# Optimization experiments

Measured on AMD Instinct MI355X. Metric: run time of the kernel, lower is better.

The kernel has to match this reference:

```python
import jax, jax.numpy as jnp
import numpy as np

EPS = 1e-5

def _sqnorm(x):
    return jnp.sum(x * x, axis=-1, keepdims=True)

def _norm(x):
    return jnp.sqrt(_sqnorm(x) + 1e-15)

def _artanh(x):
    return jnp.arctanh(jnp.clip(x, -1.0 + EPS, 1.0 - EPS))

def exp0(v):
    n = _norm(v)
    return jnp.tanh(n) * v / jnp.maximum(n, EPS)

def log0(x):
    n = jnp.clip(_norm(x), EPS, 1.0 - EPS)
    return _artanh(n) * x / n

def mob_scalar(x, r):
    n = jnp.clip(_norm(x), EPS, 1.0 - EPS)
    return jnp.tanh(r * _artanh(n)) * x / n

def mob_add(x, y):
    x2 = _sqnorm(x); y2 = _sqnorm(y)
    xy = jnp.sum(x * y, axis=-1, keepdims=True)
    num = (1.0 + 2.0 * xy + y2) * x + (1.0 - x2) * y
    den = 1.0 + 2.0 * xy + x2 * y2
    return num / jnp.maximum(den, EPS)

def pdist(x, y):
    # Poincare-ball geodesic distance, keepdims on last axis
    d2 = _sqnorm(x - y)
    den = jnp.maximum((1.0 - _sqnorm(x)) * (1.0 - _sqnorm(y)), EPS)
    return jnp.arccosh(jnp.maximum(1.0 + 2.0 * d2 / den, 1.0 + 1e-7))

def _coattention(D, Q, q1):
    # vectorized form of the per-slot loop: each slot i reads the ORIGINAL D[:, i]
    Dd = jax.lax.stop_gradient(D)                       # Zk_s is detached in torch
    # [N, F_D, F_Q, 1] attention over Q neighbors for every D slot
    G = jax.nn.softmax(-pdist(Dd[:, :, None, :], Q[:, None, :, :]), axis=2)
    nh = exp0(jnp.sum(log0(mob_scalar(Q[:, None, :, :], G)), axis=2))  # [N, F_D, d]
    return mob_add(mob_scalar(Dd, q1), nh)

def _aggregate(h_self, h_neigh, scalar):
    att = jax.nn.softmax(-pdist(h_self[:, None, :], h_neigh), axis=1)  # [N, F, 1]
    nTE = exp0(jnp.sum(log0(mob_scalar(h_neigh, att)), axis=1))        # [N, d]
    return mob_add(mob_scalar(h_self, scalar), nTE)

def _mode_forward(x, D_idx, Q_idx, emb0, emb1, win, bin_, q, qq, q1, aw1, ab1, aw2, wout, bout):
    f = jnp.concatenate([emb0[x[:, 0]], emb1[x[:, 1]]], axis=-1)  # [N, 64]
    f = exp0(f @ win + bin_)
    D = f[D_idx]; Q = f[Q_idx]                                    # [N, F, d]
    h_neigh = _coattention(D, Q, q1)
    e1 = _aggregate(f, h_neigh, q)
    e2 = _aggregate(f, Q, qq)
    z = jnp.stack([log0(e1), log0(e2)], axis=1)                   # [N, 2, d]
    beta = jax.nn.softmax(jnp.tanh(z @ aw1 + ab1) @ aw2, axis=1)  # [N, 2, 1]
    rst = exp0(jnp.sum(beta * z, axis=1))
    return exp0(log0(rst) @ wout + bout)

N, F, DH, V0, V1 = 2048, 20, 64, 100000, 1000

def setup_inputs() -> dict:
    key = jax.random.key(0)
    ks = jax.random.split(key, 32)
    def mk(k, shape, s=0.1):
        return (jax.random.normal(k, shape) * s).astype(jnp.float32)
    inp = {
        'x': jax.random.randint(ks[0], (N, 2), 0, V1).astype(jnp.int32),
        'idx_sim': jax.random.randint(ks[1], (N, F), 0, N).astype(jnp.int32),
        'idx_cor': jax.random.randint(ks[2], (N, F), 0, N).astype(jnp.int32),
    }
    for mi, m in enumerate(['sim', 'cor']):
        kk = jax.random.split(ks[3 + mi], 12)
        inp[f'emb0_{m}'] = mk(kk[0], (V0, 32))
        inp[f'emb1_{m}'] = mk(kk[1], (V1, 32))
        inp[f'win_{m}'] = mk(kk[2], (64, DH))
        inp[f'bin_{m}'] = mk(kk[3], (DH,))
        inp[f'q_{m}'] = jnp.full((1,), 0.1, jnp.float32)
        inp[f'qq_{m}'] = jnp.full((1,), 0.1, jnp.float32)
        inp[f'q1_{m}'] = jnp.full((1,), 0.1, jnp.float32)
        inp[f'aw1_{m}'] = mk(kk[4], (64, 32))
        inp[f'ab1_{m}'] = mk(kk[5], (32,))
        inp[f'aw2_{m}'] = mk(kk[6], (32, 1))
        inp[f'wout_{m}'] = mk(kk[7], (DH, 64))
        inp[f'bout_{m}'] = mk(kk[8], (64,))
    return inp

def reference(x, idx_sim, idx_cor,
              emb0_sim, emb1_sim, win_sim, bin_sim, q_sim, qq_sim, q1_sim,
              aw1_sim, ab1_sim, aw2_sim, wout_sim, bout_sim,
              emb0_cor, emb1_cor, win_cor, bin_cor, q_cor, qq_cor, q1_cor,
              aw1_cor, ab1_cor, aw2_cor, wout_cor, bout_cor):
    # mode 'sim': D = feat[idx_cor], Q = feat[idx_sim]; mode 'cor': swapped
    out_sim = _mode_forward(x, idx_cor, idx_sim, emb0_sim, emb1_sim, win_sim, bin_sim,
                            q_sim, qq_sim, q1_sim, aw1_sim, ab1_sim, aw2_sim, wout_sim, bout_sim)
    out_cor = _mode_forward(x, idx_sim, idx_cor, emb0_cor, emb1_cor, win_cor, bin_cor,
                            q_cor, qq_cor, q1_cor, aw1_cor, ab1_cor, aw2_cor, wout_cor, bout_cor)
    return jnp.stack([out_sim, out_cor], axis=0)  # [2, N, 64]
```

## Files before the change

kernel.cpp:

```cpp
#include <hip/hip_runtime.h>

#define EPS 1e-5f
#define ONE_M_EPS (1.0f - 1e-5f)
#define NROW 2048
#define FF 20
#define DH 64
#define PADW (DH + 4)
#define NPAIR (FF * FF)
#define NPAIR2 (NPAIR + FF)

typedef float v2f __attribute__((ext_vector_type(2)));

__device__ __forceinline__ float frcp(float x) { return __builtin_amdgcn_rcpf(x); }
__device__ __forceinline__ float fsq(float x) { return __builtin_amdgcn_sqrtf(x); }
__device__ __forceinline__ v2f pkfma(v2f a, v2f b, v2f c) {
  return __builtin_elementwise_fma(a, b, c);
}

template <int CTRL>
__device__ __forceinline__ float dppadd(float x) {
  int t = __builtin_amdgcn_update_dpp(0, __float_as_int(x), CTRL, 0xf, 0xf, false);
  return x + __int_as_float(t);
}
__device__ __forceinline__ float wredb(float v) {
  v = dppadd<0x111>(v);
  v = dppadd<0x112>(v);
  v = dppadd<0x114>(v);
  v = dppadd<0x118>(v);
  v = dppadd<0x142>(v);
  v = dppadd<0x143>(v);
  return __int_as_float(__builtin_amdgcn_readlane(__float_as_int(v), 63));
}

__device__ __forceinline__ float ftanh(float x) {
  float ax = fabsf(x);
  float e = __expf(-2.f * ax);
  float t = (1.f - e) * frcp(1.f + e);
  return copysignf(t, x);
}

__device__ __forceinline__ float ftanhp(float x) {
  float e = __expf(-2.f * x);
  return (1.f - e) * frcp(1.f + e);
}

__device__ __forceinline__ float fatanh(float x) {
  return 0.5f * __logf((1.f + x) * frcp(1.f - x));
}

__device__ __forceinline__ float clampn(float x) {
  return fminf(fmaxf(x, EPS), ONE_M_EPS);
}

__device__ __forceinline__ float expnacosh(float arg) {
  return frcp(arg + fsq(fmaxf(arg * arg - 1.f, 0.f)));
}

__device__ __forceinline__ float dot64(const float* __restrict__ a,
                                       const float* __restrict__ b) {
  const float4* ap = (const float4*)a;
  const float4* bp = (const float4*)b;
  v2f acc = {0.f, 0.f};
#pragma unroll
  for (int kk = 0; kk < DH / 4; ++kk) {
    float4 x = ap[kk];
    float4 y = bp[kk];
    acc = pkfma(v2f{x.x, x.y}, v2f{y.x, y.y}, acc);
    acc = pkfma(v2f{x.z, x.w}, v2f{y.z, y.w}, acc);
  }
  return acc.x + acc.y;
}

struct FeatParams {
  const float *emb0, *emb1, *win, *bin;
  float* fout;
};

struct ModeParams {
  const float* f;
  const int *Didx, *Qidx;
  const float *q1p, *qp, *qqp, *aw1, *ab1, *aw2, *wout, *bout;
  float* out;
};

__global__ __launch_bounds__(64) void feat_kernel(const int* __restrict__ x,
                                                  FeatParams ps, FeatParams pc) {
  const int bid = blockIdx.x;
  const int mode = bid >= NROW;
  const FeatParams P = mode ? pc : ps;
  const int n = bid - mode * NROW;
  const int l = threadIdx.x;
  __shared__ float u[DH];
  int x0 = x[n * 2 + 0];
  int x1 = x[n * 2 + 1];
  u[l] = (l < 32) ? P.emb0[x0 * 32 + l] : P.emb1[x1 * 32 + (l - 32)];
  __syncthreads();
  v2f acc2 = {P.bin[l], 0.f};
#pragma unroll
  for (int k = 0; k < DH; k += 2) {
    v2f uv = *(const v2f*)&u[k];
    v2f wv = {P.win[k * DH + l], P.win[(k + 1) * DH + l]};
    acc2 = pkfma(uv, wv, acc2);
  }
  float acc = acc2.x + acc2.y;
  float a2 = wredb(acc * acc);
  float nn = fsq(a2 + 1e-15f);
  P.fout[n * DH + l] = ftanhp(nn) * frcp(fmaxf(nn, EPS)) * acc;
}

__global__ __launch_bounds__(256, 4) void mode_kernel(ModeParams pm0,
                                                      ModeParams pm1) {
  const int bid = blockIdx.x;
  const int mode = bid >= NROW;
  const ModeParams P = mode ? pm1 : pm0;
  const int n = bid - mode * NROW;
  const int tid = threadIdx.x;
  const int l = tid & 63;
  const int w = tid >> 6;

  __shared__ alignas(16) float Ds[FF][PADW];
  __shared__ alignas(16) float Qs[FF][PADW];
  __shared__ alignas(16) float fs_[PADW];
  __shared__ alignas(16) float Gm[NPAIR];
  __shared__ float Fq[FF];
  __shared__ float D2[FF];
  __shared__ float FD[FF], X2s[FF];
  __shared__ float Q2[FF], WQ[FF];
  __shared__ float zb[2][DH];
  __shared__ float ub[DH];
  __shared__ float pb[4][DH];

  const float* f = P.f;
  float fv = f[n * DH + l];

  for (int i = w; i < FF; i += 4) {
    Ds[i][l] = f[P.Didx[n * FF + i] * DH + l];
    Qs[i][l] = f[P.Qidx[n * FF + i] * DH + l];
  }
  if (w == 0) fs_[l] = fv;
  float f2 = wredb(fv * fv);
  float fnc = clampn(fsq(f2 + 1e-15f));
  float fA = fatanh(fnc);
  float q1 = P.q1p[0], qsc = P.qp[0], qqsc = P.qqp[0];
  __syncthreads();

  if (w < 2 && l < FF) {
    const float* rp = (w == 0) ? &Ds[l][0] : &Qs[l][0];
    float dot = dot64(rp, rp);
    float nc = clampn(fsq(dot + 1e-15f));
    float at = fatanh(nc);
    if (w == 0) {
      D2[l] = dot;
      float fd = ftanh(q1 * at) * frcp(nc);
      FD[l] = fd;
      X2s[l] = fd * fd * dot;
    } else {
      Q2[l] = dot;
      WQ[l] = at * frcp(nc);
    }
  }
  __syncthreads();

  float qregS[FF];
#pragma unroll
  for (int j = 0; j < FF; ++j) qregS[j] = WQ[j] * Qs[j][l];

  for (int p = tid; p < NPAIR2; p += 256) {
    int i = p / FF;
    int j = p - i * FF;
    const float* ap = (i < FF) ? &Ds[i][0] : &fs_[0];
    float dot = dot64(ap, &Qs[j][0]);
    if (i < FF) {
      float d2 = D2[i] + Q2[j] - 2.f * dot;
      float den = fmaxf((1.f - D2[i]) * (1.f - Q2[j]), EPS);
      float arg = fmaxf(1.f + 2.f * d2 * frcp(den), 1.f + 1e-7f);
      Gm[p] = expnacosh(arg);
    } else {
      Fq[j] = dot;
    }
  }
  __syncthreads();

#pragma unroll 1
  for (int i = w; i < FF; i += 4) {
    const float4* gr = (const float4*)(&Gm[i * FF]);
    v2f ss2 = {0.f, 0.f};
    v2f ac2 = {0.f, 0.f};
#pragma unroll
    for (int jq = 0; jq < FF / 4; ++jq) {
      float4 g4 = gr[jq];
      ss2 += v2f{g4.x, g4.y} + v2f{g4.z, g4.w};
      ac2 = pkfma(v2f{g4.x, g4.y}, v2f{qregS[4 * jq + 0], qregS[4 * jq + 1]},
                  ac2);
      ac2 = pkfma(v2f{g4.z, g4.w}, v2f{qregS[4 * jq + 2], qregS[4 * jq + 3]},
                  ac2);
    }
    float acc = (ac2.x + ac2.y) * frcp(ss2.x + ss2.y);
    float dl = Ds[i][l];
    float a2 = wredb(acc * acc);
    float xy0 = wredb(dl * acc);
    float nn = fsq(a2 + 1e-15f);
    float ec = ftanhp(nn) * frcp(fmaxf(nn, EPS));
    float fDc = FD[i];
    float x2 = X2s[i];
    float y2 = ec * ec * a2;
    float xy = fDc * ec * xy0;
    float al = 1.f + 2.f * xy + y2;
    float be = 1.f - x2;
    float rd = frcp(fmaxf(1.f + 2.f * xy + x2 * y2, EPS));
    Ds[i][l] = (al * fDc * dl + be * ec * acc) * rd;
    float h2 = (al * al * x2 + 2.f * al * be * xy + be * be * y2) * rd * rd;
    if (l == 0) D2[i] = h2;
  }
  __syncthreads();

  if (w < 2) {
    float a1 = 0.f;
    float wh = 1.f;
    if (w == 0) {
      if (l < FF) {
        float h2 = D2[l];
        float nc = clampn(fsq(h2 + 1e-15f));
        wh = fatanh(nc) * frcp(nc);
        float dot = dot64(&fs_[0], &Ds[l][0]);
        float d2 = f2 + h2 - 2.f * dot;
        float den = fmaxf((1.f - f2) * (1.f - h2), EPS);
        float arg = fmaxf(1.f + 2.f * d2 * frcp(den), 1.f + 1e-7f);
        a1 = expnacosh(arg);
      }
    } else {
      if (l < FF) {
        float d2 = f2 + Q2[l] - 2.f * Fq[l];
        float den = fmaxf((1.f - f2) * (1.f - Q2[l]), EPS);
        float arg = fmaxf(1.f + 2.f * d2 * frcp(den), 1.f + 1e-7f);
        a1 = expnacosh(arg);
      }
    }
    float s = wredb(a1);
    float c = (l < FF) ? a1 * frcp(s) * wh : 0.f;
    float accE = 0.f;
    if (w == 0) {
#pragma unroll
      for (int j = 0; j < FF; ++j) {
        float cj = __int_as_float(__builtin_amdgcn_readlane(__float_as_int(c), j));
        accE = fmaf(cj, Ds[j][l], accE);
      }
    } else {
#pragma unroll
      for (int j = 0; j < FF; ++j) {
        float cj = __int_as_float(__builtin_amdgcn_readlane(__float_as_int(c), j));
        accE = fmaf(cj, qregS[j], accE);
      }
    }
    float a2 = wredb(accE * accE);
    float nn = fsq(a2 + 1e-15f);
    float ec = ftanhp(nn) * frcp(fmaxf(nn, EPS));
    float nTE = ec * accE;
    float r = (w == 0) ? qsc : qqsc;
    float fsc = ftanh(r * fA) * frcp(fnc);
    float xv = fsc * fv;
    float x2 = fsc * fsc * f2;
    float y2 = ec * ec * a2;
    float xy = wredb(xv * nTE);
    float al = 1.f + 2.f * xy + y2;
    float be = 1.f - x2;
    float rd = frcp(fmaxf(1.f + 2.f * xy + x2 * y2, EPS));
    float ev = (al * xv + be * nTE) * rd;
    float es = (al * al * x2 + 2.f * al * be * xy + be * be * y2) * rd * rd;
    float n1 = clampn(fsq(es + 1e-15f));
    zb[w][l] = fatanh(n1) * frcp(n1) * ev;
  }
  __syncthreads();

  if (w == 0) {
    int p_ = l >> 5, c_ = l & 31;
    v2f mm2 = {P.ab1[c_], 0.f};
#pragma unroll
    for (int k = 0; k < DH; k += 2) {
      v2f zv = *(const v2f*)&zb[p_][k];
      v2f av = {P.aw1[k * 32 + c_], P.aw1[(k + 1) * 32 + c_]};
      mm2 = pkfma(zv, av, mm2);
    }
    float tt = ftanh(mm2.x + mm2.y);
    float sr = tt * P.aw2[c_];
    sr = dppadd<0x111>(sr);
    sr = dppadd<0x112>(sr);
    sr = dppadd<0x114>(sr);
    sr = dppadd<0x118>(sr);
    sr = dppadd<0x142>(sr);
    float s0 = __int_as_float(__builtin_amdgcn_readlane(__float_as_int(sr), 31));
    float s1 = __int_as_float(__builtin_amdgcn_readlane(__float_as_int(sr), 63));
    float bm = fmaxf(s0, s1);
    float b0 = __expf(s0 - bm), b1 = __expf(s1 - bm);
    float bi = frcp(b0 + b1);
    b0 *= bi;
    b1 *= bi;
    float rv = fmaf(b0, zb[0][l], b1 * zb[1][l]);
    float r2 = wredb(rv * rv);
    float rn = fsq(r2 + 1e-15f);
    float sc = ftanhp(rn) * frcp(fmaxf(rn, EPS));
    float rst = sc * rv;
    float rr = sc * sc * r2;
    float rc = clampn(fsq(rr + 1e-15f));
    ub[l] = fatanh(rc) * frcp(rc) * rst;
  }
  __syncthreads();

  {
    v2f oo2 = {0.f, 0.f};
#pragma unroll
    for (int k = 0; k < DH / 4; k += 2) {
      int kk = w * (DH / 4) + k;
      v2f uv = *(const v2f*)&ub[kk];
      v2f wv = {P.wout[kk * DH + l], P.wout[(kk + 1) * DH + l]};
      oo2 = pkfma(uv, wv, oo2);
    }
    pb[w][l] = oo2.x + oo2.y;
  }
  __syncthreads();
  if (w == 0) {
    float oo = P.bout[l] + ((pb[0][l] + pb[1][l]) + (pb[2][l] + pb[3][l]));
    float o2 = wredb(oo * oo);
    float on = fsq(o2 + 1e-15f);
    P.out[n * DH + l] = ftanhp(on) * frcp(fmaxf(on, EPS)) * oo;
  }
}

extern "C" void kernel_launch(void* const* d_in, const int* in_sizes, int n_in,
                              void* d_out, int out_size, void* d_ws,
                              size_t ws_size, hipStream_t stream) {
  const int* x = (const int*)d_in[0];
  const int* idx_sim = (const int*)d_in[1];
  const int* idx_cor = (const int*)d_in[2];
  const float* p[2][12];
  for (int m = 0; m < 2; ++m)
    for (int k = 0; k < 12; ++k) p[m][k] = (const float*)d_in[3 + m * 12 + k];

  float* fsim = (float*)d_ws;
  float* fcor = fsim + NROW * DH;
  float* out = (float*)d_out;

  FeatParams fps = {p[0][0], p[0][1], p[0][2], p[0][3], fsim};
  FeatParams fpc = {p[1][0], p[1][1], p[1][2], p[1][3], fcor};
  feat_kernel<<<2 * NROW, 64, 0, stream>>>(x, fps, fpc);

  ModeParams m0 = {fsim, idx_cor, idx_sim, p[0][6], p[0][4], p[0][5],
                   p[0][7], p[0][8], p[0][9], p[0][10], p[0][11], out};
  ModeParams m1 = {fcor, idx_sim, idx_cor, p[1][6], p[1][4], p[1][5],
                   p[1][7], p[1][8], p[1][9], p[1][10], p[1][11], out + NROW * DH};
  mode_kernel<<<2 * NROW, 256, 0, stream>>>(m0, m1);
}
```

Before: 46.88 us.

## Shrink mode kernel to one wavefront per row

Restructures mode_kernel from 256 threads (4 wavefronts) per row to a single 64-lane wavefront. All per-row stages run serially within that one wave: gathers, norm precompute, pairwise distances, the coattention loop, both aggregations, and the output projection. Neighbor indices are loaded once and broadcast with readlane, and the cross-wave partial-sum buffer for the output matmul is removed. This lowers per-block work imbalance (two of four waves were idle in several phases) and lets more blocks share a CU. In exchange, each row's latency grows because the pairwise and per-slot loops now run sequentially in one wave.

```diff
diff --git a/kernel.cpp b/kernel.cpp
--- a/kernel.cpp
+++ b/kernel.cpp
@@ -16,6 +16,9 @@
 __device__ __forceinline__ v2f pkfma(v2f a, v2f b, v2f c) {
   return __builtin_elementwise_fma(a, b, c);
 }
+__device__ __forceinline__ float rdlane(float v, int lane) {
+  return __int_as_float(__builtin_amdgcn_readlane(__float_as_int(v), lane));
+}
 
 template <int CTRL>
 __device__ __forceinline__ float dppadd(float x) {
@@ -29,7 +32,7 @@
   v = dppadd<0x118>(v);
   v = dppadd<0x142>(v);
   v = dppadd<0x143>(v);
-  return __int_as_float(__builtin_amdgcn_readlane(__float_as_int(v), 63));
+  return rdlane(v, 63);
 }
 
 __device__ __forceinline__ float ftanh(float x) {
@@ -108,15 +111,12 @@
   P.fout[n * DH + l] = ftanhp(nn) * frcp(fmaxf(nn, EPS)) * acc;
 }
 
-__global__ __launch_bounds__(256, 4) void mode_kernel(ModeParams pm0,
-                                                      ModeParams pm1) {
+__global__ __launch_bounds__(64) void mode_kernel(ModeParams pm0, ModeParams pm1) {
   const int bid = blockIdx.x;
   const int mode = bid >= NROW;
   const ModeParams P = mode ? pm1 : pm0;
   const int n = bid - mode * NROW;
-  const int tid = threadIdx.x;
-  const int l = tid & 63;
-  const int w = tid >> 6;
+  const int l = threadIdx.x;
 
   __shared__ alignas(16) float Ds[FF][PADW];
   __shared__ alignas(16) float Qs[FF][PADW];
@@ -128,35 +128,41 @@
   __shared__ float Q2[FF], WQ[FF];
   __shared__ float zb[2][DH];
   __shared__ float ub[DH];
-  __shared__ float pb[4][DH];
 
   const float* f = P.f;
   float fv = f[n * DH + l];
 
-  for (int i = w; i < FF; i += 4) {
-    Ds[i][l] = f[P.Didx[n * FF + i] * DH + l];
-    Qs[i][l] = f[P.Qidx[n * FF + i] * DH + l];
-  }
-  if (w == 0) fs_[l] = fv;
+  int di = (l < FF) ? P.Didx[n * FF + l] : 0;
+  int qi = (l < FF) ? P.Qidx[n * FF + l] : 0;
+#pragma unroll
+  for (int i = 0; i < FF; ++i) {
+    int ri = __builtin_amdgcn_readlane(di, i);
+    int rq = __builtin_amdgcn_readlane(qi, i);
+    Ds[i][l] = f[ri * DH + l];
+    Qs[i][l] = f[rq * DH + l];
+  }
+  fs_[l] = fv;
   float f2 = wredb(fv * fv);
   float fnc = clampn(fsq(f2 + 1e-15f));
   float fA = fatanh(fnc);
   float q1 = P.q1p[0], qsc = P.qp[0], qqsc = P.qqp[0];
   __syncthreads();
 
-  if (w < 2 && l < FF) {
-    const float* rp = (w == 0) ? &Ds[l][0] : &Qs[l][0];
+  {
+    const bool isD = (l < FF);
+    const bool isQ = (l >= 32 && l < 32 + FF);
+    const float* rp = isD ? &Ds[l][0] : (isQ ? &Qs[l - 32][0] : &fs_[0]);
     float dot = dot64(rp, rp);
     float nc = clampn(fsq(dot + 1e-15f));
     float at = fatanh(nc);
-    if (w == 0) {
+    if (isD) {
       D2[l] = dot;
       float fd = ftanh(q1 * at) * frcp(nc);
       FD[l] = fd;
       X2s[l] = fd * fd * dot;
-    } else {
-      Q2[l] = dot;
-      WQ[l] = at * frcp(nc);
+    } else if (isQ) {
+      Q2[l - 32] = dot;
+      WQ[l - 32] = at * frcp(nc);
     }
   }
   __syncthreads();
@@ -165,7 +171,7 @@
 #pragma unroll
   for (int j = 0; j < FF; ++j) qregS[j] = WQ[j] * Qs[j][l];
 
-  for (int p = tid; p < NPAIR2; p += 256) {
+  for (int p = l; p < NPAIR2; p += 64) {
     int i = p / FF;
     int j = p - i * FF;
     const float* ap = (i < FF) ? &Ds[i][0] : &fs_[0];
@@ -182,7 +188,7 @@
   __syncthreads();
 
 #pragma unroll 1
-  for (int i = w; i < FF; i += 4) {
+  for (int i = 0; i < FF; ++i) {
     const float4* gr = (const float4*)(&Gm[i * FF]);
     v2f ss2 = {0.f, 0.f};
     v2f ac2 = {0.f, 0.f};
@@ -214,10 +220,11 @@
   }
   __syncthreads();
 
-  if (w < 2) {
+#pragma unroll
+  for (int m = 0; m < 2; ++m) {
     float a1 = 0.f;
     float wh = 1.f;
-    if (w == 0) {
+    if (m == 0) {
       if (l < FF) {
         float h2 = D2[l];
         float nc = clampn(fsq(h2 + 1e-15f));
@@ -239,24 +246,18 @@
     float s = wredb(a1);
     float c = (l < FF) ? a1 * frcp(s) * wh : 0.f;
     float accE = 0.f;
-    if (w == 0) {
-#pragma unroll
-      for (int j = 0; j < FF; ++j) {
-        float cj = __int_as_float(__builtin_amdgcn_readlane(__float_as_int(c), j));
-        accE = fmaf(cj, Ds[j][l], accE);
-      }
+    if (m == 0) {
+#pragma unroll
+      for (int j = 0; j < FF; ++j) accE = fmaf(rdlane(c, j), Ds[j][l], accE);
     } else {
 #pragma unroll
-      for (int j = 0; j < FF; ++j) {
-        float cj = __int_as_float(__builtin_amdgcn_readlane(__float_as_int(c), j));
-        accE = fmaf(cj, qregS[j], accE);
-      }
+      for (int j = 0; j < FF; ++j) accE = fmaf(rdlane(c, j), qregS[j], accE);
     }
     float a2 = wredb(accE * accE);
     float nn = fsq(a2 + 1e-15f);
     float ec = ftanhp(nn) * frcp(fmaxf(nn, EPS));
     float nTE = ec * accE;
-    float r = (w == 0) ? qsc : qqsc;
+    float r = (m == 0) ? qsc : qqsc;
     float fsc = ftanh(r * fA) * frcp(fnc);
     float xv = fsc * fv;
     float x2 = fsc * fsc * f2;
@@ -268,11 +269,11 @@
     float ev = (al * xv + be * nTE) * rd;
     float es = (al * al * x2 + 2.f * al * be * xy + be * be * y2) * rd * rd;
     float n1 = clampn(fsq(es + 1e-15f));
-    zb[w][l] = fatanh(n1) * frcp(n1) * ev;
-  }
-  __syncthreads();
-
-  if (w == 0) {
+    zb[m][l] = fatanh(n1) * frcp(n1) * ev;
+  }
+  __syncthreads();
+
+  {
     int p_ = l >> 5, c_ = l & 31;
     v2f mm2 = {P.ab1[c_], 0.f};
 #pragma unroll
@@ -288,8 +289,8 @@
     sr = dppadd<0x114>(sr);
     sr = dppadd<0x118>(sr);
     sr = dppadd<0x142>(sr);
-    float s0 = __int_as_float(__builtin_amdgcn_readlane(__float_as_int(sr), 31));
-    float s1 = __int_as_float(__builtin_amdgcn_readlane(__float_as_int(sr), 63));
+    float s0 = rdlane(sr, 31);
+    float s1 = rdlane(sr, 63);
     float bm = fmaxf(s0, s1);
     float b0 = __expf(s0 - bm), b1 = __expf(s1 - bm);
     float bi = frcp(b0 + b1);
@@ -309,17 +310,12 @@
   {
     v2f oo2 = {0.f, 0.f};
 #pragma unroll
-    for (int k = 0; k < DH / 4; k += 2) {
-      int kk = w * (DH / 4) + k;
-      v2f uv = *(const v2f*)&ub[kk];
-      v2f wv = {P.wout[kk * DH + l], P.wout[(kk + 1) * DH + l]};
+    for (int k = 0; k < DH; k += 2) {
+      v2f uv = *(const v2f*)&ub[k];
+      v2f wv = {P.wout[k * DH + l], P.wout[(k + 1) * DH + l]};
       oo2 = pkfma(uv, wv, oo2);
     }
-    pb[w][l] = oo2.x + oo2.y;
-  }
-  __syncthreads();
-  if (w == 0) {
-    float oo = P.bout[l] + ((pb[0][l] + pb[1][l]) + (pb[2][l] + pb[3][l]));
+    float oo = P.bout[l] + oo2.x + oo2.y;
     float o2 = wredb(oo * oo);
     float on = fsq(o2 + 1e-15f);
     P.out[n * DH + l] = ftanhp(on) * frcp(fmaxf(on, EPS)) * oo;
@@ -348,5 +344,5 @@
                    p[0][7], p[0][8], p[0][9], p[0][10], p[0][11], out};
   ModeParams m1 = {fcor, idx_sim, idx_cor, p[1][6], p[1][4], p[1][5],
                    p[1][7], p[1][8], p[1][9], p[1][10], p[1][11], out + NROW * DH};
-  mode_kernel<<<2 * NROW, 256, 0, stream>>>(m0, m1);
-}
+  mode_kernel<<<2 * NROW, 64, 0, stream>>>(m0, m1);
+}
```

After: 48.70 us. 3.9% more time.

## Batch coattention norm reductions per row into one wave via shared staging

Applied to the files above, without the earlier changes.

The per-slot loop that did two 64-lane wave reductions per D slot is split into phases. The attention-weighted sums are staged into shared memory (reusing the Qs buffer, which is no longer needed at that point), then wave 0 computes every slot's squared norm and cross dot product lane-parallel and writes per-slot Möbius coefficients and the log-map weight. A final elementwise pass updates Ds. The launch-bounds occupancy hint is also dropped, which frees register pressure for the fully unrolled loop, and a readlane helper is added for tidiness. In exchange the kernel gains two more block barriers and leaves three of the four waves idle during the coefficient step.

```diff
diff --git a/kernel.cpp b/kernel.cpp
--- a/kernel.cpp
+++ b/kernel.cpp
@@ -16,6 +16,9 @@
 __device__ __forceinline__ v2f pkfma(v2f a, v2f b, v2f c) {
   return __builtin_elementwise_fma(a, b, c);
 }
+__device__ __forceinline__ float rdlane(float v, int lane) {
+  return __int_as_float(__builtin_amdgcn_readlane(__float_as_int(v), lane));
+}
 
 template <int CTRL>
 __device__ __forceinline__ float dppadd(float x) {
@@ -29,7 +32,7 @@
   v = dppadd<0x118>(v);
   v = dppadd<0x142>(v);
   v = dppadd<0x143>(v);
-  return __int_as_float(__builtin_amdgcn_readlane(__float_as_int(v), 63));
+  return rdlane(v, 63);
 }
 
 __device__ __forceinline__ float ftanh(float x) {
@@ -108,8 +111,8 @@
   P.fout[n * DH + l] = ftanhp(nn) * frcp(fmaxf(nn, EPS)) * acc;
 }
 
-__global__ __launch_bounds__(256, 4) void mode_kernel(ModeParams pm0,
-                                                      ModeParams pm1) {
+__global__ __launch_bounds__(256) void mode_kernel(ModeParams pm0,
+                                                   ModeParams pm1) {
   const int bid = blockIdx.x;
   const int mode = bid >= NROW;
   const ModeParams P = mode ? pm1 : pm0;
@@ -126,9 +129,12 @@
   __shared__ float D2[FF];
   __shared__ float FD[FF], X2s[FF];
   __shared__ float Q2[FF], WQ[FF];
+  __shared__ float C1[FF], C2[FF], WH[FF];
   __shared__ float zb[2][DH];
   __shared__ float ub[DH];
   __shared__ float pb[4][DH];
+
+  float (*As)[PADW] = Qs;
 
   const float* f = P.f;
   float fv = f[n * DH + l];
@@ -181,8 +187,10 @@
   }
   __syncthreads();
 
-#pragma unroll 1
-  for (int i = w; i < FF; i += 4) {
+  float acc5[5];
+#pragma unroll
+  for (int s = 0; s < 5; ++s) {
+    const int i = w + 4 * s;
     const float4* gr = (const float4*)(&Gm[i * FF]);
     v2f ss2 = {0.f, 0.f};
     v2f ac2 = {0.f, 0.f};
@@ -196,21 +204,44 @@
                   ac2);
     }
     float acc = (ac2.x + ac2.y) * frcp(ss2.x + ss2.y);
-    float dl = Ds[i][l];
-    float a2 = wredb(acc * acc);
-    float xy0 = wredb(dl * acc);
-    float nn = fsq(a2 + 1e-15f);
-    float ec = ftanhp(nn) * frcp(fmaxf(nn, EPS));
-    float fDc = FD[i];
-    float x2 = X2s[i];
-    float y2 = ec * ec * a2;
-    float xy = fDc * ec * xy0;
-    float al = 1.f + 2.f * xy + y2;
-    float be = 1.f - x2;
-    float rd = frcp(fmaxf(1.f + 2.f * xy + x2 * y2, EPS));
-    Ds[i][l] = (al * fDc * dl + be * ec * acc) * rd;
-    float h2 = (al * al * x2 + 2.f * al * be * xy + be * be * y2) * rd * rd;
-    if (l == 0) D2[i] = h2;
+    acc5[s] = acc;
+    As[i][l] = acc;
+  }
+  __syncthreads();
+
+  if (w == 0) {
+    const bool isA = (l < FF);
+    const bool isX = (l >= 32 && l < 32 + FF);
+    const float* pa = isA ? &As[l][0] : (isX ? &As[l - 32][0] : &fs_[0]);
+    const float* pc2 = isA ? &As[l][0] : (isX ? &Ds[l - 32][0] : &fs_[0]);
+    float dotv = dot64(pa, pc2);
+    float xyv = __shfl(dotv, l + 32, 64);
+    if (isA) {
+      float a2 = dotv;
+      float xy0 = xyv;
+      float nn = fsq(a2 + 1e-15f);
+      float ec = ftanhp(nn) * frcp(fmaxf(nn, EPS));
+      float fDc = FD[l];
+      float x2 = X2s[l];
+      float y2 = ec * ec * a2;
+      float xy = fDc * ec * xy0;
+      float al = 1.f + 2.f * xy + y2;
+      float be = 1.f - x2;
+      float rd = frcp(fmaxf(1.f + 2.f * xy + x2 * y2, EPS));
+      C1[l] = al * fDc * rd;
+      C2[l] = be * ec * rd;
+      float h2 = (al * al * x2 + 2.f * al * be * xy + be * be * y2) * rd * rd;
+      D2[l] = h2;
+      float nc = clampn(fsq(h2 + 1e-15f));
+      WH[l] = fatanh(nc) * frcp(nc);
+    }
+  }
+  __syncthreads();
+
+#pragma unroll
+  for (int s = 0; s < 5; ++s) {
+    const int i = w + 4 * s;
+    Ds[i][l] = fmaf(C1[i], Ds[i][l], C2[i] * acc5[s]);
   }
   __syncthreads();
 
@@ -220,8 +251,7 @@
     if (w == 0) {
       if (l < FF) {
         float h2 = D2[l];
-        float nc = clampn(fsq(h2 + 1e-15f));
-        wh = fatanh(nc) * frcp(nc);
+        wh = WH[l];
         float dot = dot64(&fs_[0], &Ds[l][0]);
         float d2 = f2 + h2 - 2.f * dot;
         float den = fmaxf((1.f - f2) * (1.f - h2), EPS);
@@ -241,16 +271,10 @@
     float accE = 0.f;
     if (w == 0) {
 #pragma unroll
-      for (int j = 0; j < FF; ++j) {
-        float cj = __int_as_float(__builtin_amdgcn_readlane(__float_as_int(c), j));
-        accE = fmaf(cj, Ds[j][l], accE);
-      }
+      for (int j = 0; j < FF; ++j) accE = fmaf(rdlane(c, j), Ds[j][l], accE);
     } else {
 #pragma unroll
-      for (int j = 0; j < FF; ++j) {
-        float cj = __int_as_float(__builtin_amdgcn_readlane(__float_as_int(c), j));
-        accE = fmaf(cj, qregS[j], accE);
-      }
+      for (int j = 0; j < FF; ++j) accE = fmaf(rdlane(c, j), qregS[j], accE);
     }
     float a2 = wredb(accE * accE);
     float nn = fsq(a2 + 1e-15f);
@@ -288,8 +312,8 @@
     sr = dppadd<0x114>(sr);
     sr = dppadd<0x118>(sr);
     sr = dppadd<0x142>(sr);
-    float s0 = __int_as_float(__builtin_amdgcn_readlane(__float_as_int(sr), 31));
-    float s1 = __int_as_float(__builtin_amdgcn_readlane(__float_as_int(sr), 63));
+    float s0 = rdlane(sr, 31);
+    float s1 = rdlane(sr, 63);
     float bm = fmaxf(s0, s1);
     float b0 = __expf(s0 - bm), b1 = __expf(s1 - bm);
     float bi = frcp(b0 + b1);
```

Result: faster. 42.61 us (-9.1%).
